# Kernel tuning notes

Hardware: AMD Instinct MI355X
Metric: run time of the kernel (lower is better)

## Reference

```python
import jax, jax.numpy as jnp
import numpy as np

IMAGE_SIZE = 1024
DOWNSIZING = 64
THRESHOLD = 0.65  # default_threshold_target (threshold arg == 0)
NUM_BG_POINTS = 1
ORI_SHAPE = (2160, 3840)
EMBED_C, FEAT_H, FEAT_W = 256, 64, 64


def setup_inputs() -> dict:
    key = jax.random.key(0)
    k1, k2 = jax.random.split(key)
    image_embeddings = jax.random.normal(k1, (1, EMBED_C, FEAT_H, FEAT_W), dtype=jnp.float32)
    reference_feat = jax.random.normal(k2, (1, EMBED_C), dtype=jnp.float32) * 0.1
    ori_shape = jnp.array(ORI_SHAPE, dtype=jnp.int32)
    return {"image_embeddings": image_embeddings, "reference_feat": reference_feat, "ori_shape": ori_shape}


def _postprocess_masks(sim, H, W):
    # F.interpolate to (image_size, image_size), crop to pre-padded size, resize to ori_shape
    sim = jax.image.resize(sim, (1, 1, IMAGE_SIZE, IMAGE_SIZE), method="bilinear", antialias=False)
    scale = IMAGE_SIZE / max(H, W)
    ph = int(np.floor(H * scale + 0.5))
    pw = int(np.floor(W * scale + 0.5))
    sim = sim[..., :ph, :pw]
    return jax.image.resize(sim, (1, 1, H, W), method="bilinear", antialias=False)


def reference(image_embeddings, reference_feat, ori_shape):
    H, W = int(ori_shape[0]), int(ori_shape[1])
    # --- similarity map ---
    t = image_embeddings[0]                                   # (C, hf, wf)
    c, hf, wf = t.shape
    t = t / jnp.linalg.norm(t, axis=0, keepdims=True)         # channel-wise L2 norm
    sim = (reference_feat @ t.reshape(c, hf * wf)).reshape(1, 1, hf, wf)
    sim = _postprocess_masks(sim, H, W)
    m = sim[0, 0]                                             # (H, W)
    flat = m.reshape(-1)                                      # (H*W,)
    hw = H * W

    # --- background points: k smallest values ---
    _, bg_idx = jax.lax.top_k(-flat, NUM_BG_POINTS)
    bg_row = bg_idx // W
    bg_col = bg_idx % W
    bg_coords = jnp.stack([bg_col, bg_row], axis=1).astype(jnp.float32)  # (N, 2) = (x, y)

    # --- foreground points: grid-binned per-cell max (segment-max form of
    #     torch.where + unique + broadcast-equality + per-bin topk) ---
    ratio = IMAGE_SIZE / max(H, W)
    n_cells_side = IMAGE_SIZE // DOWNSIZING                    # 16; bounds grid rows/cols
    num_cells = n_cells_side * n_cells_side                    # 256 fixed
    idx = jnp.arange(hw, dtype=jnp.int32)
    ys = idx // W
    xs = idx % W
    gy = jnp.floor(ys * (ratio / DOWNSIZING)).astype(jnp.int32)
    gx = jnp.floor(xs * (ratio / DOWNSIZING)).astype(jnp.int32)
    seg = gy * n_cells_side + gx                               # grid id per pixel

    valid = flat > THRESHOLD
    masked = jnp.where(valid, flat, -jnp.inf)
    seg_max = jax.ops.segment_max(masked, seg, num_segments=num_cells)
    # first pixel achieving the cell max (matches torch.topk tie behavior)
    is_max = valid & (masked == seg_max[seg])
    cand = jnp.where(is_max, idx, hw)
    best = jax.ops.segment_min(cand, seg, num_segments=num_cells)
    cell_valid = best < hw
    bi = jnp.minimum(best, hw - 1)
    px = (bi % W).astype(jnp.float32)
    py = (bi // W).astype(jnp.float32)
    ps = flat[bi]
    points = jnp.stack([px, py, ps], axis=1)                   # (num_cells, 3) = (x, y, score)
    points = jnp.where(cell_valid[:, None], points, -1.0)      # mimic F.pad(value=-1) rows
    sort_key = jnp.where(cell_valid, ps, -jnp.inf)
    order = jnp.argsort(-sort_key)                             # score descending, invalid last
    points_scores = points[order]
    return points_scores, bg_coords
```

## Files before the change

kernel.cpp:

```cpp
#include <hip/hip_runtime.h>

#define W_OUT 3840
#define H_OUT 2160
#define IW 1024
#define IH 576

__device__ __forceinline__ unsigned int enc_f32(float f) {
    unsigned int b = __float_as_uint(f);
    return b ^ (0x80000000u | (unsigned int)((int)b >> 31));
}

__global__ __launch_bounds__(256) void sim_kernel(
    const float* __restrict__ emb, const float* __restrict__ ref,
    float* __restrict__ sim)
{
    const int lane = threadIdx.x & 63;
    const int wave = threadIdx.x >> 6;
    const int p = blockIdx.x * 64 + lane;
    const int cbase = wave * 64;
    float dot = 0.f, ss = 0.f;
#pragma unroll 8
    for (int cc = 0; cc < 64; ++cc) {
        int c = cbase + cc;
        float a = emb[c * 4096 + p];
        dot = fmaf(ref[c], a, dot);
        ss  = fmaf(a, a, ss);
    }
    __shared__ float sdot[4][64];
    __shared__ float sss[4][64];
    sdot[wave][lane] = dot;
    sss[wave][lane]  = ss;
    __syncthreads();
    if (wave == 0) {
        float d = (sdot[0][lane] + sdot[1][lane]) + (sdot[2][lane] + sdot[3][lane]);
        float s = (sss[0][lane] + sss[1][lane]) + (sss[2][lane] + sss[3][lane]);
        sim[p] = d / sqrtf(s);
    }
}

__global__ __launch_bounds__(256) void scan_kernel(
    const float* __restrict__ sim,
    unsigned long long* __restrict__ cellPart,
    unsigned long long* __restrict__ bgPart)
{
    __shared__ float4 I4[2][IW / 4];
    __shared__ unsigned long long wmin[4];
    float* I0 = (float*)&I4[0][0];
    float* I1 = (float*)&I4[1][0];

    const float INV375 = (float)(1.0 / 3.75);
    const float INV16  = 0.0625f;

    const int y   = blockIdx.x;
    const int tid = threadIdx.x;

    float fy  = ((float)y + 0.5f) * INV375 - 0.5f;
    float fyf = floorf(fy);
    float wy  = fy - fyf;
    int ai = (int)fyf;
    int a1 = min(max(ai + 1, 0), IH - 1);
    int a0 = min(max(ai,     0), IH - 1);

    for (int r = 0; r < 2; ++r) {
        int a = (r == 0) ? a0 : a1;
        float fa  = ((float)a + 0.5f) * INV16 - 0.5f;
        float faf = floorf(fa);
        float wa  = fa - faf;
        int si = (int)faf;
        int s1 = min(max(si + 1, 0), 63);
        int s0 = min(max(si,     0), 63);
        const float* row0 = sim + s0 * 64;
        const float* row1 = sim + s1 * 64;
        float* dst = (r == 0) ? I0 : I1;
        for (int b = tid; b < IW; b += 256) {
            float fb  = ((float)b + 0.5f) * INV16 - 0.5f;
            float fbf = floorf(fb);
            float wb  = fb - fbf;
            int ci = (int)fbf;
            int c1 = min(max(ci + 1, 0), 63);
            int c0 = min(max(ci,     0), 63);
            float v0 = row0[c0] * (1.f - wb) + row0[c1] * wb;
            float v1 = row1[c0] * (1.f - wb) + row1[c1] * wb;
            dst[b] = v0 * (1.f - wa) + v1 * wa;
        }
    }
    __syncthreads();

    unsigned long long bestCell = 0ull;
    unsigned long long bestBg   = 0xFFFFFFFFFFFFFFFFull;
    const int x0 = tid * 15;
    const unsigned int idxBase = (unsigned int)(y * W_OUT + x0);

#define UPD(F, jj) {                                                        \
        unsigned long long top = ((unsigned long long)enc_f32(F)) << 32;    \
        unsigned int idx = idxBase + (jj);                                  \
        unsigned long long bgk = top | (unsigned long long)idx;             \
        unsigned long long ck  = top | (unsigned long long)(~idx);          \
        if (ck  > bestCell) bestCell = ck;                                  \
        if (bgk < bestBg)   bestBg   = bgk;                                 \
    }

    if (tid == 0 || tid == 255) {
#pragma unroll
        for (int j = 0; j < 15; ++j) {
            int x = x0 + j;
            float fx  = ((float)x + 0.5f) * INV375 - 0.5f;
            float fxf = floorf(fx);
            float wx  = fx - fxf;
            int bi = (int)fxf;
            int b1 = min(max(bi + 1, 0), IW - 1);
            int b0 = min(max(bi,     0), IW - 1);
            float v0 = I0[b0] * (1.f - wx) + I0[b1] * wx;
            float v1 = I1[b0] * (1.f - wx) + I1[b1] * wx;
            float F  = v0 * (1.f - wy) + v1 * wy;
            UPD(F, j)
        }
    } else {
        float4 A0 = I4[0][tid - 1], B0 = I4[0][tid], C0 = I4[0][tid + 1];
        float4 A1 = I4[1][tid - 1], B1 = I4[1][tid], C1 = I4[1][tid + 1];
        const float rr0[12] = {A0.x,A0.y,A0.z,A0.w, B0.x,B0.y,B0.z,B0.w, C0.x,C0.y,C0.z,C0.w};
        const float rr1[12] = {A1.x,A1.y,A1.z,A1.w, B1.x,B1.y,B1.z,B1.w, C1.x,C1.y,C1.z,C1.w};

#define PX(j, i0) {                                                         \
            float fx  = ((float)(x0 + (j)) + 0.5f) * INV375 - 0.5f;         \
            float fxf = floorf(fx);                                         \
            float wx  = fx - fxf;                                           \
            float v0 = rr0[(i0)] * (1.f - wx) + rr0[(i0) + 1] * wx;         \
            float v1 = rr1[(i0)] * (1.f - wx) + rr1[(i0) + 1] * wx;         \
            float F  = v0 * (1.f - wy) + v1 * wy;                           \
            UPD(F, j)                                                       \
        }
        PX(0,3)  PX(1,3)  PX(2,4)  PX(3,4)  PX(4,4)
        PX(5,4)  PX(6,5)  PX(7,5)  PX(8,5)  PX(9,6)
        PX(10,6) PX(11,6) PX(12,6) PX(13,7) PX(14,7)
#undef PX
    }
#undef UPD

#pragma unroll
    for (int m = 1; m <= 8; m <<= 1) {
        unsigned long long o = __shfl_xor(bestCell, m, 64);
        if (o > bestCell) bestCell = o;
    }
    if ((tid & 15) == 0) cellPart[y * 16 + (tid >> 4)] = bestCell;

#pragma unroll
    for (int m = 1; m <= 32; m <<= 1) {
        unsigned long long o = __shfl_xor(bestBg, m, 64);
        if (o < bestBg) bestBg = o;
    }
    if ((tid & 63) == 0) wmin[tid >> 6] = bestBg;
    __syncthreads();
    if (tid == 0) {
        unsigned long long b0 = wmin[0] < wmin[1] ? wmin[0] : wmin[1];
        unsigned long long b1 = wmin[2] < wmin[3] ? wmin[2] : wmin[3];
        bgPart[y] = b0 < b1 ? b0 : b1;
    }
}

__global__ __launch_bounds__(256) void finalize_kernel(
    const unsigned long long* __restrict__ cellPart,
    const unsigned long long* __restrict__ bgPart,
    float* __restrict__ out)
{
    __shared__ float sk[256];
    __shared__ unsigned long long sb[256];
    const int t = threadIdx.x;

    unsigned long long best = 0ull;
    if (t < 144) {
        const int band = t >> 4, cx = t & 15;
        const unsigned long long* p = cellPart + (band * 240) * 16 + cx;
#pragma unroll 8
        for (int r = 0; r < 240; ++r) {
            unsigned long long k = p[r * 16];
            if (k > best) best = k;
        }
    }
    float px = -1.f, py = -1.f, ps = -1.f;
    float key = -__builtin_huge_valf();
    if (best != 0ull) {
        unsigned int e = (unsigned int)(best >> 32);
        unsigned int b = (e & 0x80000000u) ? (e ^ 0x80000000u) : ~e;
        float v = __uint_as_float(b);
        if (v > 0.65f) {
            unsigned int idx = ~((unsigned int)(best & 0xFFFFFFFFull));
            px = (float)(idx % W_OUT);
            py = (float)(idx / W_OUT);
            ps = v;
            key = v;
        }
    }

    unsigned long long m = 0xFFFFFFFFFFFFFFFFull;
    for (int i = t; i < H_OUT; i += 256) {
        unsigned long long k = bgPart[i];
        if (k < m) m = k;
    }
    sb[t] = m;
    __syncthreads();
    for (int s = 128; s > 0; s >>= 1) {
        if (t < s) {
            unsigned long long o = sb[t + s];
            if (o < sb[t]) sb[t] = o;
        }
        __syncthreads();
    }

    sk[t] = key;
    __syncthreads();
    int rank = 0;
    for (int j = 0; j < 256; ++j) {
        float kj = sk[j];
        if (kj > key || (kj == key && j < t)) rank++;
    }
    out[rank * 3 + 0] = px;
    out[rank * 3 + 1] = py;
    out[rank * 3 + 2] = ps;
    if (t == 0) {
        unsigned int idx = (unsigned int)(sb[0] & 0xFFFFFFFFull);
        out[256 * 3 + 0] = (float)(idx % W_OUT);
        out[256 * 3 + 1] = (float)(idx / W_OUT);
    }
}

extern "C" void kernel_launch(void* const* d_in, const int* in_sizes, int n_in,
                              void* d_out, int out_size, void* d_ws, size_t ws_size,
                              hipStream_t stream) {
    (void)in_sizes; (void)n_in; (void)out_size; (void)ws_size;
    const float* emb = (const float*)d_in[0];
    const float* ref = (const float*)d_in[1];
    float* out = (float*)d_out;

    float* sim = (float*)d_ws;
    unsigned long long* cellPart = (unsigned long long*)((char*)d_ws + 16384);
    unsigned long long* bgPart   = cellPart + H_OUT * 16;

    sim_kernel<<<64, 256, 0, stream>>>(emb, ref, sim);
    scan_kernel<<<H_OUT, 256, 0, stream>>>(sim, cellPart, bgPart);
    finalize_kernel<<<1, 256, 0, stream>>>(cellPart, bgPart, out);
}
```

Measured before the change: 98.36 us.

## Fuse finalize into scan kernel via atomic reductions and last-block pattern

Per-row partial results are now reduced with 64-bit atomicMax/atomicMin into a 144-entry cell table and a single background minimum, instead of being written to large per-row arrays. The last block to finish, detected with a global atomic counter, performs the ranking and output writes, so the separate finalize kernel launch goes away. The sim kernel now also initializes the atomic table and counter. This saves one kernel launch and the serial scan over the partial arrays, in exchange for atomic contention on the shared cells and a thread fence in every block.

```diff
diff --git a/kernel.cpp b/kernel.cpp
--- a/kernel.cpp
+++ b/kernel.cpp
@@ -12,8 +12,17 @@
 
 __global__ __launch_bounds__(256) void sim_kernel(
     const float* __restrict__ emb, const float* __restrict__ ref,
-    float* __restrict__ sim)
+    float* __restrict__ sim,
+    unsigned long long* __restrict__ cellTab,
+    unsigned long long* __restrict__ bgMin,
+    unsigned int* __restrict__ counter)
 {
+    if (blockIdx.x == 0) {
+        const int t = threadIdx.x;
+        if (t < 144)        cellTab[t] = 0ull;
+        else if (t == 144)  *bgMin = 0xFFFFFFFFFFFFFFFFull;
+        else if (t == 145)  *counter = 0u;
+    }
     const int lane = threadIdx.x & 63;
     const int wave = threadIdx.x >> 6;
     const int p = blockIdx.x * 64 + lane;
@@ -40,11 +49,15 @@
 
 __global__ __launch_bounds__(256) void scan_kernel(
     const float* __restrict__ sim,
-    unsigned long long* __restrict__ cellPart,
-    unsigned long long* __restrict__ bgPart)
+    unsigned long long* __restrict__ cellTab,
+    unsigned long long* __restrict__ bgMin,
+    unsigned int* __restrict__ counter,
+    float* __restrict__ out)
 {
     __shared__ float4 I4[2][IW / 4];
     __shared__ unsigned long long wmin[4];
+    __shared__ unsigned int lastFlag;
+    __shared__ float sk[256];
     float* I0 = (float*)&I4[0][0];
     float* I1 = (float*)&I4[1][0];
 
@@ -142,7 +155,8 @@
         unsigned long long o = __shfl_xor(bestCell, m, 64);
         if (o > bestCell) bestCell = o;
     }
-    if ((tid & 15) == 0) cellPart[y * 16 + (tid >> 4)] = bestCell;
+    if ((tid & 15) == 0)
+        atomicMax(cellTab + (y / 240) * 16 + (tid >> 4), bestCell);
 
 #pragma unroll
     for (int m = 1; m <= 32; m <<= 1) {
@@ -154,57 +168,32 @@
     if (tid == 0) {
         unsigned long long b0 = wmin[0] < wmin[1] ? wmin[0] : wmin[1];
         unsigned long long b1 = wmin[2] < wmin[3] ? wmin[2] : wmin[3];
-        bgPart[y] = b0 < b1 ? b0 : b1;
-    }
-}
-
-__global__ __launch_bounds__(256) void finalize_kernel(
-    const unsigned long long* __restrict__ cellPart,
-    const unsigned long long* __restrict__ bgPart,
-    float* __restrict__ out)
-{
-    __shared__ float sk[256];
-    __shared__ unsigned long long sb[256];
-    const int t = threadIdx.x;
-
-    unsigned long long best = 0ull;
-    if (t < 144) {
-        const int band = t >> 4, cx = t & 15;
-        const unsigned long long* p = cellPart + (band * 240) * 16 + cx;
-#pragma unroll 8
-        for (int r = 0; r < 240; ++r) {
-            unsigned long long k = p[r * 16];
-            if (k > best) best = k;
-        }
-    }
+        atomicMin(bgMin, b0 < b1 ? b0 : b1);
+        __threadfence();
+        unsigned int old = atomicAdd(counter, 1u);
+        lastFlag = (old == (unsigned int)(H_OUT - 1)) ? 1u : 0u;
+    }
+    __syncthreads();
+    if (!lastFlag) return;
+
+    const int t = tid;
+
     float px = -1.f, py = -1.f, ps = -1.f;
     float key = -__builtin_huge_valf();
-    if (best != 0ull) {
-        unsigned int e = (unsigned int)(best >> 32);
-        unsigned int b = (e & 0x80000000u) ? (e ^ 0x80000000u) : ~e;
-        float v = __uint_as_float(b);
-        if (v > 0.65f) {
-            unsigned int idx = ~((unsigned int)(best & 0xFFFFFFFFull));
-            px = (float)(idx % W_OUT);
-            py = (float)(idx / W_OUT);
-            ps = v;
-            key = v;
-        }
-    }
-
-    unsigned long long m = 0xFFFFFFFFFFFFFFFFull;
-    for (int i = t; i < H_OUT; i += 256) {
-        unsigned long long k = bgPart[i];
-        if (k < m) m = k;
-    }
-    sb[t] = m;
-    __syncthreads();
-    for (int s = 128; s > 0; s >>= 1) {
-        if (t < s) {
-            unsigned long long o = sb[t + s];
-            if (o < sb[t]) sb[t] = o;
-        }
-        __syncthreads();
+    if (t < 144) {
+        unsigned long long best = atomicMax(cellTab + t, 0ull);
+        if (best != 0ull) {
+            unsigned int e = (unsigned int)(best >> 32);
+            unsigned int b = (e & 0x80000000u) ? (e ^ 0x80000000u) : ~e;
+            float v = __uint_as_float(b);
+            if (v > 0.65f) {
+                unsigned int idx = ~((unsigned int)(best & 0xFFFFFFFFull));
+                px = (float)(idx % W_OUT);
+                py = (float)(idx / W_OUT);
+                ps = v;
+                key = v;
+            }
+        }
     }
 
     sk[t] = key;
@@ -218,7 +207,8 @@
     out[rank * 3 + 1] = py;
     out[rank * 3 + 2] = ps;
     if (t == 0) {
-        unsigned int idx = (unsigned int)(sb[0] & 0xFFFFFFFFull);
+        unsigned long long bg = atomicMin(bgMin, 0xFFFFFFFFFFFFFFFFull);
+        unsigned int idx = (unsigned int)(bg & 0xFFFFFFFFull);
         out[256 * 3 + 0] = (float)(idx % W_OUT);
         out[256 * 3 + 1] = (float)(idx / W_OUT);
     }
@@ -233,10 +223,10 @@
     float* out = (float*)d_out;
 
     float* sim = (float*)d_ws;
-    unsigned long long* cellPart = (unsigned long long*)((char*)d_ws + 16384);
-    unsigned long long* bgPart   = cellPart + H_OUT * 16;
-
-    sim_kernel<<<64, 256, 0, stream>>>(emb, ref, sim);
-    scan_kernel<<<H_OUT, 256, 0, stream>>>(sim, cellPart, bgPart);
-    finalize_kernel<<<1, 256, 0, stream>>>(cellPart, bgPart, out);
-}
+    unsigned long long* cellTab = (unsigned long long*)((char*)d_ws + 16384);
+    unsigned long long* bgMin   = (unsigned long long*)((char*)d_ws + 16384 + 144 * 8);
+    unsigned int*       counter = (unsigned int*)((char*)d_ws + 16384 + 144 * 8 + 8);
+
+    sim_kernel<<<64, 256, 0, stream>>>(emb, ref, sim, cellTab, bgMin, counter);
+    scan_kernel<<<H_OUT, 256, 0, stream>>>(sim, cellTab, bgMin, counter, out);
+}
```

New measurement: 129.3 us. 1.31x slower.
